# Optimization experiments

Hardware: AMD Instinct MI355X
Metric: run time of the kernel (lower is better)

## Reference

```python
import jax, jax.numpy as jnp
import numpy as np

B, I, H1, H2, E, T = 16384, 512, 256, 128, 8, 2


def setup_inputs() -> dict:
    key = jax.random.key(0)
    ks = jax.random.split(key, 4)
    # Xavier-ish scaling for stability
    x = jax.random.normal(ks[0], (B, I), dtype=jnp.float32)
    W1 = jax.random.normal(ks[1], (E, I, H1), dtype=jnp.float32) / np.sqrt(I)
    b1 = jnp.zeros((E, H1), dtype=jnp.float32)
    W2 = jax.random.normal(ks[2], (E, H1, H2), dtype=jnp.float32) / np.sqrt(H1)
    b2 = jnp.zeros((E, H2), dtype=jnp.float32)
    Wg = jax.random.normal(ks[3], (T, I, E), dtype=jnp.float32) / np.sqrt(I)
    bg = jnp.zeros((T, E), dtype=jnp.float32)
    return {"x": x, "W1": W1, "b1": b1, "W2": W2, "b2": b2, "Wg": Wg, "bg": bg}


def reference(x, W1, b1, W2, b2, Wg, bg):
    # All experts as one grouped GEMM: [E, B, H1]
    h = jax.nn.relu(jnp.einsum('bi,eih->ebh', x, W1) + b1[:, None, :])
    # Last expert layer (lastlayer_reg=True -> act applied): [E, B, H2]
    e_out = jax.nn.relu(jnp.einsum('ebh,eho->ebo', h, W2) + b2[:, None, :])
    # Per-task gates with softmax over experts: [T, B, E]
    gates = jax.nn.softmax(jnp.einsum('bi,tie->tbe', x, Wg) + bg[:, None, :], axis=-1)
    # Gate-weighted combine of expert outputs: [T, B, H2]
    towers = jnp.einsum('tbe,ebo->tbo', gates, e_out)
    return towers
```

## Files before the change

kernel.cpp:

```cpp
#include <hip/hip_runtime.h>
#include <hip/hip_bf16.h>

#define B_  16384
#define I_  512
#define H1_ 256
#define H2_ 128
#define E_  8
#define T_  2

typedef __attribute__((ext_vector_type(8))) short short8;
typedef __attribute__((ext_vector_type(4))) float float4_t;

__device__ inline unsigned short f2bf(float f) {
    union { float f; unsigned u; } v; v.f = f;
    unsigned r = v.u + 0x7FFFu + ((v.u >> 16) & 1u);
    return (unsigned short)(r >> 16);
}

__device__ inline void async_copy16(const unsigned short* g, unsigned short* l) {
    __builtin_amdgcn_global_load_lds(
        (const __attribute__((address_space(1))) void*)g,
        (__attribute__((address_space(3))) void*)l,
        16, 0, 0);
}

__global__ void conv_x_kernel(const float* __restrict__ x, unsigned short* __restrict__ xb) {
    int idx = blockIdx.x * 256 + threadIdx.x;
    size_t base = (size_t)idx * 8;
    float4_t a = *(const float4_t*)(x + base);
    float4_t b = *(const float4_t*)(x + base + 4);
    short8 s;
    s[0] = (short)f2bf(a[0]); s[1] = (short)f2bf(a[1]);
    s[2] = (short)f2bf(a[2]); s[3] = (short)f2bf(a[3]);
    s[4] = (short)f2bf(b[0]); s[5] = (short)f2bf(b[1]);
    s[6] = (short)f2bf(b[2]); s[7] = (short)f2bf(b[3]);
    *(short8*)(xb + base) = s;
}

__global__ void transpose_bf16_kernel(const float* __restrict__ in, unsigned short* __restrict__ out,
                                      int R, int C) {
    __shared__ float tile[32][33];
    int e = blockIdx.z;
    int c0 = blockIdx.x * 32;
    int r0 = blockIdx.y * 32;
    const float* inp = in + (size_t)e * R * C;
    unsigned short* outp = out + (size_t)e * R * C;
    int tx = threadIdx.x, ty = threadIdx.y;
#pragma unroll
    for (int j = 0; j < 32; j += 8)
        tile[ty + j][tx] = inp[(size_t)(r0 + ty + j) * C + c0 + tx];
    __syncthreads();
#pragma unroll
    for (int j = 0; j < 32; j += 8)
        outp[(size_t)(c0 + ty + j) * R + r0 + tx] = f2bf(tile[tx][ty + j]);
}

__global__ void prep_wgt_kernel(const float* __restrict__ wg, unsigned short* __restrict__ wgt) {
    int idx = blockIdx.x * 256 + threadIdx.x;
    int te = idx >> 9;
    int i  = idx & 511;
    int t = te >> 3, e = te & 7;
    wgt[(size_t)te * I_ + i] = f2bf(wg[(size_t)t * I_ * E_ + (size_t)i * E_ + e]);
}

__global__ void gates_kernel(const unsigned short* __restrict__ xb,
                             const unsigned short* __restrict__ wgt,
                             const float* __restrict__ bg,
                             float* __restrict__ gates) {
    int w = threadIdx.x >> 6, lane = threadIdx.x & 63;
    int row0 = (blockIdx.x * 4 + w) * 16;
    int col = lane & 15, quad = lane >> 4;
    float4_t acc = {0.f, 0.f, 0.f, 0.f};
    const unsigned short* aG = xb + (size_t)(row0 + col) * I_ + quad * 8;
    const unsigned short* bG = wgt + (size_t)col * I_ + quad * 8;
#pragma unroll
    for (int k = 0; k < I_; k += 32) {
        short8 a = *(const short8*)(aG + k);
        short8 b = *(const short8*)(bG + k);
        acc = __builtin_amdgcn_mfma_f32_16x16x32_bf16(a, b, acc, 0, 0, 0);
    }
    float bias = bg[col];
#pragma unroll
    for (int p = 0; p < 4; ++p) {
        float v = acc[p] + bias;
        float m = v;
        m = fmaxf(m, __shfl_xor(m, 1));
        m = fmaxf(m, __shfl_xor(m, 2));
        m = fmaxf(m, __shfl_xor(m, 4));
        float ev = __expf(v - m);
        float s = ev;
        s += __shfl_xor(s, 1);
        s += __shfl_xor(s, 2);
        s += __shfl_xor(s, 4);
        gates[(size_t)col * B_ + row0 + quad * 4 + p] = ev / s;
    }
}

__global__ void gemm_relu_kernel(const unsigned short* __restrict__ A, size_t aSE,
                                 const unsigned short* __restrict__ Bt, size_t bSE,
                                 const float* __restrict__ bias, int biasSE,
                                 unsigned short* __restrict__ C, size_t cSE,
                                 int K, int lda, int ldb, int ldc) {
    __shared__ unsigned short As[128 * 64];
    __shared__ unsigned short Bs[128 * 64];
    int e = blockIdx.z;
    const unsigned short* Ae = A + (size_t)e * aSE;
    const unsigned short* Be = Bt + (size_t)e * bSE;
    const float* biasE = bias + (size_t)e * biasSE;
    unsigned short* Ce = C + (size_t)e * cSE;
    int m0 = blockIdx.x * 128, n0 = blockIdx.y * 128;
    int t = threadIdx.x, w = t >> 6, lane = t & 63;
    int col = lane & 15, quad = lane >> 4;
    int wm = (w & 1) * 64, wn = (w >> 1) * 64;

    float4_t acc[4][4];
#pragma unroll
    for (int mi = 0; mi < 4; ++mi)
#pragma unroll
        for (int ni = 0; ni < 4; ++ni)
            acc[mi][ni] = (float4_t){0.f, 0.f, 0.f, 0.f};

    int rT = t >> 3;
    int gk = (((t & 7) ^ (rT & 7))) * 8;
    const unsigned short* aG = Ae + (size_t)(m0 + rT) * lda + gk;
    const unsigned short* bG = Be + (size_t)(n0 + rT) * ldb + gk;
    unsigned short* aL = As + (size_t)w * 64 * 8;
    unsigned short* bL = Bs + (size_t)w * 64 * 8;

    for (int k0 = 0; k0 < K; k0 += 64) {
#pragma unroll
        for (int j = 0; j < 4; ++j) {
            async_copy16(aG + (size_t)j * 32 * lda + k0, aL + j * 2048);
            async_copy16(bG + (size_t)j * 32 * ldb + k0, bL + j * 2048);
        }
        __syncthreads();
#pragma unroll
        for (int kk = 0; kk < 64; kk += 32) {
            int q = (kk >> 3) + quad;
            short8 af[4], bf[4];
#pragma unroll
            for (int mi = 0; mi < 4; ++mi) {
                int r = wm + mi * 16 + col;
                af[mi] = *(const short8*)&As[r * 64 + ((q ^ (r & 7)) * 8)];
            }
#pragma unroll
            for (int ni = 0; ni < 4; ++ni) {
                int r = wn + ni * 16 + col;
                bf[ni] = *(const short8*)&Bs[r * 64 + ((q ^ (r & 7)) * 8)];
            }
#pragma unroll
            for (int mi = 0; mi < 4; ++mi)
#pragma unroll
                for (int ni = 0; ni < 4; ++ni)
                    acc[mi][ni] = __builtin_amdgcn_mfma_f32_16x16x32_bf16(af[mi], bf[ni], acc[mi][ni], 0, 0, 0);
        }
        __syncthreads();
    }

#pragma unroll
    for (int ni = 0; ni < 4; ++ni) {
        int c = n0 + wn + ni * 16 + col;
        float bv = biasE[c];
#pragma unroll
        for (int mi = 0; mi < 4; ++mi) {
            int rbase = m0 + wm + mi * 16 + quad * 4;
#pragma unroll
            for (int p = 0; p < 4; ++p) {
                float v = acc[mi][ni][p] + bv;
                v = v > 0.f ? v : 0.f;
                Ce[(size_t)(rbase + p) * ldc + c] = f2bf(v);
            }
        }
    }
}

__global__ void fused_l2_combine_kernel(const unsigned short* __restrict__ h,
                                        const unsigned short* __restrict__ w2t,
                                        const float* __restrict__ b2,
                                        const float* __restrict__ gates,
                                        float* __restrict__ out) {
    __shared__ unsigned short As[64 * 64];
    __shared__ unsigned short Bs[128 * 64];
    __shared__ float gL[16 * 64];

    int b0 = blockIdx.x * 64;
    int t = threadIdx.x, w = t >> 6, lane = t & 63;
    int col = lane & 15, quad = lane >> 4;
    int wn = w * 32;

    {
        int te = t >> 4, i4 = (t & 15) * 4;
        *(float4_t*)&gL[te * 64 + i4] = *(const float4_t*)&gates[(size_t)te * B_ + b0 + i4];
    }

    float4_t tw0[4][2], tw1[4][2];
#pragma unroll
    for (int mi = 0; mi < 4; ++mi)
#pragma unroll
        for (int ni = 0; ni < 2; ++ni) {
            tw0[mi][ni] = (float4_t){0.f, 0.f, 0.f, 0.f};
            tw1[mi][ni] = (float4_t){0.f, 0.f, 0.f, 0.f};
        }

    int rT = t >> 3;
    int slot = t & 7;

    for (int e = 0; e < E_; ++e) {
        const unsigned short* hE = h + (size_t)e * B_ * H1_;
        const unsigned short* w2E = w2t + (size_t)e * H2_ * H1_;

        float4_t acc[4][2];
#pragma unroll
        for (int mi = 0; mi < 4; ++mi)
#pragma unroll
            for (int ni = 0; ni < 2; ++ni)
                acc[mi][ni] = (float4_t){0.f, 0.f, 0.f, 0.f};

        for (int k0 = 0; k0 < H1_; k0 += 64) {
#pragma unroll
            for (int j = 0; j < 2; ++j) {
                int row = j * 32 + rT;
                int gk = (slot ^ (row & 7)) * 8;
                async_copy16(hE + (size_t)(b0 + row) * H1_ + k0 + gk,
                             As + j * 2048 + w * 512);
            }
#pragma unroll
            for (int j = 0; j < 4; ++j) {
                int row = j * 32 + rT;
                int gk = (slot ^ (row & 7)) * 8;
                async_copy16(w2E + (size_t)row * H1_ + k0 + gk,
                             Bs + j * 2048 + w * 512);
            }
            __syncthreads();
#pragma unroll
            for (int kk = 0; kk < 64; kk += 32) {
                int q = (kk >> 3) + quad;
                short8 af[4], bfr[2];
#pragma unroll
                for (int mi = 0; mi < 4; ++mi) {
                    int r = mi * 16 + col;
                    af[mi] = *(const short8*)&As[r * 64 + ((q ^ (r & 7)) * 8)];
                }
#pragma unroll
                for (int ni = 0; ni < 2; ++ni) {
                    int r = wn + ni * 16 + col;
                    bfr[ni] = *(const short8*)&Bs[r * 64 + ((q ^ (r & 7)) * 8)];
                }
#pragma unroll
                for (int mi = 0; mi < 4; ++mi)
#pragma unroll
                    for (int ni = 0; ni < 2; ++ni)
                        acc[mi][ni] = __builtin_amdgcn_mfma_f32_16x16x32_bf16(af[mi], bfr[ni], acc[mi][ni], 0, 0, 0);
            }
            __syncthreads();
        }

        float bv0 = b2[e * H2_ + wn + col];
        float bv1 = b2[e * H2_ + wn + 16 + col];
#pragma unroll
        for (int mi = 0; mi < 4; ++mi) {
            float4_t g0 = *(const float4_t*)&gL[e * 64 + mi * 16 + quad * 4];
            float4_t g1 = *(const float4_t*)&gL[(8 + e) * 64 + mi * 16 + quad * 4];
#pragma unroll
            for (int ni = 0; ni < 2; ++ni) {
                float bv = ni == 0 ? bv0 : bv1;
#pragma unroll
                for (int p = 0; p < 4; ++p) {
                    float v = acc[mi][ni][p] + bv;
                    v = v > 0.f ? v : 0.f;
                    tw0[mi][ni][p] += g0[p] * v;
                    tw1[mi][ni][p] += g1[p] * v;
                }
            }
        }
    }

#pragma unroll
    for (int mi = 0; mi < 4; ++mi) {
#pragma unroll
        for (int ni = 0; ni < 2; ++ni) {
            int n = wn + ni * 16 + col;
#pragma unroll
            for (int p = 0; p < 4; ++p) {
                int r = b0 + mi * 16 + quad * 4 + p;
                out[(size_t)r * H2_ + n] = tw0[mi][ni][p];
                out[(size_t)B_ * H2_ + (size_t)r * H2_ + n] = tw1[mi][ni][p];
            }
        }
    }
}

extern "C" void kernel_launch(void* const* d_in, const int* in_sizes, int n_in,
                              void* d_out, int out_size, void* d_ws, size_t ws_size,
                              hipStream_t stream) {
    const float* x  = (const float*)d_in[0];
    const float* W1 = (const float*)d_in[1];
    const float* b1 = (const float*)d_in[2];
    const float* W2 = (const float*)d_in[3];
    const float* b2 = (const float*)d_in[4];
    const float* Wg = (const float*)d_in[5];
    const float* bg = (const float*)d_in[6];
    float* out = (float*)d_out;

    char* ws = (char*)d_ws;
    unsigned short* xb    = (unsigned short*)(ws);
    unsigned short* w1t   = (unsigned short*)(ws + 16777216);
    unsigned short* w2t   = (unsigned short*)(ws + 18874368);
    unsigned short* wgt   = (unsigned short*)(ws + 19398656);
    float*          gates = (float*)(ws + 19415040);
    unsigned short* h     = (unsigned short*)(ws + 20463616);

    conv_x_kernel<<<dim3(B_ * I_ / 8 / 256), 256, 0, stream>>>(x, xb);
    transpose_bf16_kernel<<<dim3(H1_ / 32, I_ / 32, E_), dim3(32, 8), 0, stream>>>(W1, w1t, I_, H1_);
    transpose_bf16_kernel<<<dim3(H2_ / 32, H1_ / 32, E_), dim3(32, 8), 0, stream>>>(W2, w2t, H1_, H2_);
    prep_wgt_kernel<<<dim3(T_ * E_ * I_ / 256), 256, 0, stream>>>(Wg, wgt);

    gates_kernel<<<dim3(B_ / 64), 256, 0, stream>>>(xb, wgt, bg, gates);

    gemm_relu_kernel<<<dim3(B_ / 128, H1_ / 128, E_), 256, 0, stream>>>(
        xb, 0, w1t, (size_t)H1_ * I_, b1, H1_, h, (size_t)B_ * H1_, I_, I_, I_, H1_);

    fused_l2_combine_kernel<<<dim3(B_ / 64), 256, 0, stream>>>(h, w2t, b2, gates, out);
}
```

Measured before the change: 183.7 us.

## Fuse x bf16 conversion into gates kernel and retile layer-2 combine kernel

Removes the standalone x-to-bf16 conversion kernel. The gates kernel now reads fp32 x, converts it in registers, feeds the MFMA and writes the bf16 copy for the later GEMM, which saves one launch and one full read of x. The fused layer-2/combine kernel switches to 32-row batch tiles with a 128-wide K step, which doubles the grid and halves the sync count per expert. In exchange, each block reloads the W2 tile for fewer rows, and the LDS footprint grows to about 40 KB.

```diff
diff --git a/kernel.cpp b/kernel.cpp
--- a/kernel.cpp
+++ b/kernel.cpp
@@ -22,19 +22,6 @@
         (const __attribute__((address_space(1))) void*)g,
         (__attribute__((address_space(3))) void*)l,
         16, 0, 0);
-}
-
-__global__ void conv_x_kernel(const float* __restrict__ x, unsigned short* __restrict__ xb) {
-    int idx = blockIdx.x * 256 + threadIdx.x;
-    size_t base = (size_t)idx * 8;
-    float4_t a = *(const float4_t*)(x + base);
-    float4_t b = *(const float4_t*)(x + base + 4);
-    short8 s;
-    s[0] = (short)f2bf(a[0]); s[1] = (short)f2bf(a[1]);
-    s[2] = (short)f2bf(a[2]); s[3] = (short)f2bf(a[3]);
-    s[4] = (short)f2bf(b[0]); s[5] = (short)f2bf(b[1]);
-    s[6] = (short)f2bf(b[2]); s[7] = (short)f2bf(b[3]);
-    *(short8*)(xb + base) = s;
 }
 
 __global__ void transpose_bf16_kernel(const float* __restrict__ in, unsigned short* __restrict__ out,
@@ -63,19 +50,28 @@
     wgt[(size_t)te * I_ + i] = f2bf(wg[(size_t)t * I_ * E_ + (size_t)i * E_ + e]);
 }
 
-__global__ void gates_kernel(const unsigned short* __restrict__ xb,
-                             const unsigned short* __restrict__ wgt,
-                             const float* __restrict__ bg,
-                             float* __restrict__ gates) {
+__global__ void gates_conv_kernel(const float* __restrict__ x,
+                                  unsigned short* __restrict__ xb,
+                                  const unsigned short* __restrict__ wgt,
+                                  const float* __restrict__ bg,
+                                  float* __restrict__ gates) {
     int w = threadIdx.x >> 6, lane = threadIdx.x & 63;
     int row0 = (blockIdx.x * 4 + w) * 16;
     int col = lane & 15, quad = lane >> 4;
     float4_t acc = {0.f, 0.f, 0.f, 0.f};
-    const unsigned short* aG = xb + (size_t)(row0 + col) * I_ + quad * 8;
+    const float* xr = x + (size_t)(row0 + col) * I_ + quad * 8;
+    unsigned short* xbr = xb + (size_t)(row0 + col) * I_ + quad * 8;
     const unsigned short* bG = wgt + (size_t)col * I_ + quad * 8;
 #pragma unroll
     for (int k = 0; k < I_; k += 32) {
-        short8 a = *(const short8*)(aG + k);
+        float4_t xa = *(const float4_t*)(xr + k);
+        float4_t xc = *(const float4_t*)(xr + k + 4);
+        short8 a;
+        a[0] = (short)f2bf(xa[0]); a[1] = (short)f2bf(xa[1]);
+        a[2] = (short)f2bf(xa[2]); a[3] = (short)f2bf(xa[3]);
+        a[4] = (short)f2bf(xc[0]); a[5] = (short)f2bf(xc[1]);
+        a[6] = (short)f2bf(xc[2]); a[7] = (short)f2bf(xc[3]);
+        *(short8*)(xbr + k) = a;
         short8 b = *(const short8*)(bG + k);
         acc = __builtin_amdgcn_mfma_f32_16x16x32_bf16(a, b, acc, 0, 0, 0);
     }
@@ -179,75 +175,77 @@
                                         const float* __restrict__ b2,
                                         const float* __restrict__ gates,
                                         float* __restrict__ out) {
-    __shared__ unsigned short As[64 * 64];
-    __shared__ unsigned short Bs[128 * 64];
-    __shared__ float gL[16 * 64];
-
-    int b0 = blockIdx.x * 64;
+    __shared__ unsigned short As[32 * 128];
+    __shared__ unsigned short Bs[128 * 128];
+    __shared__ float gL[16 * 32];
+
+    int b0 = blockIdx.x * 32;
     int t = threadIdx.x, w = t >> 6, lane = t & 63;
     int col = lane & 15, quad = lane >> 4;
     int wn = w * 32;
 
-    {
-        int te = t >> 4, i4 = (t & 15) * 4;
-        *(float4_t*)&gL[te * 64 + i4] = *(const float4_t*)&gates[(size_t)te * B_ + b0 + i4];
-    }
-
-    float4_t tw0[4][2], tw1[4][2];
-#pragma unroll
-    for (int mi = 0; mi < 4; ++mi)
+    if (t < 128) {
+        int te = t >> 3, i4 = (t & 7) * 4;
+        *(float4_t*)&gL[te * 32 + i4] = *(const float4_t*)&gates[(size_t)te * B_ + b0 + i4];
+    }
+
+    float4_t tw0[2][2], tw1[2][2];
+#pragma unroll
+    for (int mi = 0; mi < 2; ++mi)
 #pragma unroll
         for (int ni = 0; ni < 2; ++ni) {
             tw0[mi][ni] = (float4_t){0.f, 0.f, 0.f, 0.f};
             tw1[mi][ni] = (float4_t){0.f, 0.f, 0.f, 0.f};
         }
 
-    int rT = t >> 3;
-    int slot = t & 7;
+    int rT = t >> 4;
+    int slot = t & 15;
 
     for (int e = 0; e < E_; ++e) {
         const unsigned short* hE = h + (size_t)e * B_ * H1_;
         const unsigned short* w2E = w2t + (size_t)e * H2_ * H1_;
 
-        float4_t acc[4][2];
-#pragma unroll
-        for (int mi = 0; mi < 4; ++mi)
+        float4_t acc[2][2];
+#pragma unroll
+        for (int mi = 0; mi < 2; ++mi)
 #pragma unroll
             for (int ni = 0; ni < 2; ++ni)
                 acc[mi][ni] = (float4_t){0.f, 0.f, 0.f, 0.f};
 
-        for (int k0 = 0; k0 < H1_; k0 += 64) {
+        for (int k0 = 0; k0 < H1_; k0 += 128) {
 #pragma unroll
             for (int j = 0; j < 2; ++j) {
-                int row = j * 32 + rT;
-                int gk = (slot ^ (row & 7)) * 8;
+                int row = j * 16 + rT;
+                int gk = (((slot ^ row) & 7) | (slot & 8)) * 8;
                 async_copy16(hE + (size_t)(b0 + row) * H1_ + k0 + gk,
                              As + j * 2048 + w * 512);
             }
 #pragma unroll
-            for (int j = 0; j < 4; ++j) {
-                int row = j * 32 + rT;
-                int gk = (slot ^ (row & 7)) * 8;
+            for (int j = 0; j < 8; ++j) {
+                int row = j * 16 + rT;
+                int gk = (((slot ^ row) & 7) | (slot & 8)) * 8;
                 async_copy16(w2E + (size_t)row * H1_ + k0 + gk,
                              Bs + j * 2048 + w * 512);
             }
             __syncthreads();
 #pragma unroll
-            for (int kk = 0; kk < 64; kk += 32) {
+            for (int kk = 0; kk < 128; kk += 32) {
                 int q = (kk >> 3) + quad;
-                short8 af[4], bfr[2];
-#pragma unroll
-                for (int mi = 0; mi < 4; ++mi) {
+                short8 af[2], bfr[2];
+#pragma unroll
+                for (int mi = 0; mi < 2; ++mi) {
                     int r = mi * 16 + col;
-                    af[mi] = *(const short8*)&As[r * 64 + ((q ^ (r & 7)) * 8)];
+                    int sw = ((q & 8) | ((q ^ r) & 7)) * 8;
+                    af[mi] = *(const short8*)&As[r * 128 + sw];
                 }
 #pragma unroll
                 for (int ni = 0; ni < 2; ++ni) {
                     int r = wn + ni * 16 + col;
-                    bfr[ni] = *(const short8*)&Bs[r * 64 + ((q ^ (r & 7)) * 8)];
+                    int sw = ((q & 8) | ((q ^ r) & 7)) * 8;
+                    bfr[ni] = *(const short8*)&Bs[r * 128 + sw];
                 }
 #pragma unroll
-                for (int mi = 0; mi < 4; ++mi)
+                for (int mi = 0; mi < 2; ++mi)
 #pragma unroll
                     for (int ni = 0; ni < 2; ++ni)
                         acc[mi][ni] = __builtin_amdgcn_mfma_f32_16x16x32_bf16(af[mi], bfr[ni], acc[mi][ni], 0, 0, 0);
@@ -255,15 +253,13 @@
             __syncthreads();
         }
 
-        float bv0 = b2[e * H2_ + wn + col];
-        float bv1 = b2[e * H2_ + wn + 16 + col];
-#pragma unroll
-        for (int mi = 0; mi < 4; ++mi) {
-            float4_t g0 = *(const float4_t*)&gL[e * 64 + mi * 16 + quad * 4];
-            float4_t g1 = *(const float4_t*)&gL[(8 + e) * 64 + mi * 16 + quad * 4];
+#pragma unroll
+        for (int mi = 0; mi < 2; ++mi) {
+            float4_t g0 = *(const float4_t*)&gL[e * 32 + mi * 16 + quad * 4];
+            float4_t g1 = *(const float4_t*)&gL[(8 + e) * 32 + mi * 16 + quad * 4];
 #pragma unroll
             for (int ni = 0; ni < 2; ++ni) {
-                float bv = ni == 0 ? bv0 : bv1;
+                float bv = b2[e * H2_ + wn + ni * 16 + col];
 #pragma unroll
                 for (int p = 0; p < 4; ++p) {
                     float v = acc[mi][ni][p] + bv;
@@ -276,7 +272,7 @@
     }
 
 #pragma unroll
-    for (int mi = 0; mi < 4; ++mi) {
+    for (int mi = 0; mi < 2; ++mi) {
 #pragma unroll
         for (int ni = 0; ni < 2; ++ni) {
             int n = wn + ni * 16 + col;
@@ -310,15 +306,14 @@
     float*          gates = (float*)(ws + 19415040);
     unsigned short* h     = (unsigned short*)(ws + 20463616);
 
-    conv_x_kernel<<<dim3(B_ * I_ / 8 / 256), 256, 0, stream>>>(x, xb);
     transpose_bf16_kernel<<<dim3(H1_ / 32, I_ / 32, E_), dim3(32, 8), 0, stream>>>(W1, w1t, I_, H1_);
     transpose_bf16_kernel<<<dim3(H2_ / 32, H1_ / 32, E_), dim3(32, 8), 0, stream>>>(W2, w2t, H1_, H2_);
     prep_wgt_kernel<<<dim3(T_ * E_ * I_ / 256), 256, 0, stream>>>(Wg, wgt);
 
-    gates_kernel<<<dim3(B_ / 64), 256, 0, stream>>>(xb, wgt, bg, gates);
+    gates_conv_kernel<<<dim3(B_ / 64), 256, 0, stream>>>(x, xb, wgt, bg, gates);
 
     gemm_relu_kernel<<<dim3(B_ / 128, H1_ / 128, E_), 256, 0, stream>>>(
         xb, 0, w1t, (size_t)H1_ * I_, b1, H1_, h, (size_t)B_ * H1_, I_, I_, I_, H1_);
 
-    fused_l2_combine_kernel<<<dim3(B_ / 64), 256, 0, stream>>>(h, w2t, b2, gates, out);
-}
+    fused_l2_combine_kernel<<<dim3(B_ / 32), 256, 0, stream>>>(h, w2t, b2, gates, out);
+}
```

Measured after the change: 172.9 us. 1.06x faster.
